# Performance work log

Hardware: AMD Instinct MI355X
Metric: run time of the kernel (lower is better)

## Reference

```python
import jax, jax.numpy as jnp
import numpy as np
from jax import lax

B, C, H, W = 8, 64, 128, 128
K = 3  # deformable kernel size, padding=1, stride=1


def conv3x3(x, w, b=None):
    # x: [B,Cin,H,W], w: [Cout,Cin,3,3]
    y = lax.conv_general_dilated(x, w, (1, 1), 'SAME',
                                 dimension_numbers=('NCHW', 'OIHW', 'NCHW'))
    if b is not None:
        y = y + b[None, :, None, None]
    return y


def leaky_relu(x, slope=0.1):
    return jnp.where(x >= 0, x, slope * x)


def _bilinear_sample_one(feat, ys, xs):
    # feat: [C,H,W]; ys, xs: [KK,H,W] fractional sample coords (zero outside borders)
    h, w = feat.shape[1], feat.shape[2]
    y0 = jnp.floor(ys)
    x0 = jnp.floor(xs)
    wy = ys - y0  # [KK,H,W]
    wx = xs - x0

    def gather(yi, xi):
        valid = ((yi >= 0) & (yi < h) & (xi >= 0) & (xi < w)).astype(feat.dtype)
        yc = jnp.clip(yi, 0, h - 1).astype(jnp.int32)
        xc = jnp.clip(xi, 0, w - 1).astype(jnp.int32)
        v = feat[:, yc, xc]  # [C,KK,H,W]
        return v * valid[None]

    v00 = gather(y0, x0)
    v01 = gather(y0, x0 + 1)
    v10 = gather(y0 + 1, x0)
    v11 = gather(y0 + 1, x0 + 1)
    top = v00 * (1 - wx)[None] + v01 * wx[None]
    bot = v10 * (1 - wx)[None] + v11 * wx[None]
    return top * (1 - wy)[None] + bot * wy[None]  # [C,KK,H,W]


def deform_conv2d(x, offset, weight):
    # x: [B,Cin,H,W]; offset: [B,2*K*K,H,W] (torchvision order: per-tap (dy,dx));
    # weight: [Cout,Cin,K,K]; stride=1, pad=1, dilation=1, groups=1, no bias.
    b, cin, h, w = x.shape
    kk = K * K
    off = offset.reshape(b, kk, 2, h, w)
    dy, dx = off[:, :, 0], off[:, :, 1]  # [B,KK,H,W]
    hh = jnp.arange(h, dtype=x.dtype)[:, None]
    ww = jnp.arange(w, dtype=x.dtype)[None, :]
    ky = (jnp.arange(kk) // K - 1).astype(x.dtype)[None, :, None, None]
    kx = (jnp.arange(kk) % K - 1).astype(x.dtype)[None, :, None, None]
    ys = hh[None, None] + ky + dy  # [B,KK,H,W]
    xs = ww[None, None] + kx + dx
    sampled = jax.vmap(_bilinear_sample_one)(x, ys, xs)  # [B,Cin,KK,H,W]
    wflat = weight.reshape(weight.shape[0], cin, kk)
    return jnp.einsum('bckhw,ock->bohw', sampled, wflat)


def setup_inputs() -> dict:
    key = jax.random.key(0)
    ks = jax.random.split(key, 7)
    ref_feat = jax.random.normal(ks[0], (B, C, H, W), jnp.float32)
    target_feat = jax.random.normal(ks[1], (B, C, H, W), jnp.float32)
    w1 = jax.random.normal(ks[2], (C, 2 * C, 3, 3), jnp.float32) * 0.02
    b1 = jax.random.normal(ks[3], (C,), jnp.float32) * 0.02
    w2 = jax.random.normal(ks[4], (18, C, 3, 3), jnp.float32) * 0.02
    b2 = jax.random.normal(ks[5], (18,), jnp.float32) * 0.02
    wd = jax.random.normal(ks[6], (C, C, 3, 3), jnp.float32) * 0.05
    return {'ref_feat': ref_feat, 'target_feat': target_feat,
            'w1': w1, 'b1': b1, 'w2': w2, 'b2': b2, 'wd': wd}


def reference(ref_feat, target_feat, w1, b1, w2, b2, wd):
    concat_feat = jnp.concatenate([ref_feat, target_feat], axis=1)  # [B,2C,H,W]
    hmid = leaky_relu(conv3x3(concat_feat, w1, b1), 0.1)
    offset = conv3x3(hmid, w2, b2)  # [B,18,H,W]
    aligned_feat = deform_conv2d(target_feat, offset, wd)  # [B,C,H,W]
    return aligned_feat
```

## Files before the change

### kernel.cpp

```cpp
#include <hip/hip_runtime.h>
#include <hip/hip_fp16.h>

#define HW 128
#define PLANE (HW * HW)

typedef __attribute__((ext_vector_type(8))) _Float16 f16x8;
typedef __attribute__((ext_vector_type(4))) float f32x4;

__device__ __forceinline__ unsigned short f2h(float f) {
  return __half_as_ushort(__float2half(f));
}

__device__ __forceinline__ void tile_from_bid_512(int bid, int& b, int& by, int& bx) {
  int wg = (bid & 7) * 64 + (bid >> 3);
  b = wg >> 6;
  int t = wg & 63;
  by = (t >> 3) << 4;
  bx = (t & 7) << 4;
}

__global__ __launch_bounds__(256) void pack_all_kernel(
    const float* __restrict__ w1, const float* __restrict__ w2,
    const float* __restrict__ wd, unsigned short* __restrict__ w1p,
    unsigned short* __restrict__ w2p, unsigned short* __restrict__ wdp) {
  int idx = blockIdx.x * 256 + threadIdx.x;
  if (idx < 73728) {
    int k = idx >> 6, n = idx & 63;
    int tap = k >> 7, ic = k & 127;
    w1p[((k >> 3) * 64 + n) * 8 + (k & 7)] = f2h(w1[(n * 128 + ic) * 9 + tap]);
  } else if (idx < 73728 + 18432) {
    int i = idx - 73728;
    int k = i >> 5, n = i & 31;
    int tap = k >> 6, ic = k & 63;
    float v = (n < 18) ? w2[(n * 64 + ic) * 9 + tap] : 0.f;
    w2p[((k >> 3) * 32 + n) * 8 + (k & 7)] = f2h(v);
  } else if (idx < 73728 + 18432 + 36864) {
    int i = idx - 73728 - 18432;
    int k = i >> 6, n = i & 63;
    int tap = k >> 6, ic = k & 63;
    wdp[((k >> 3) * 64 + n) * 8 + (k & 7)] = f2h(wd[(n * 64 + ic) * 9 + tap]);
  }
}

__global__ __launch_bounds__(256) void to_nhwc_kernel(
    const float* __restrict__ ref, const float* __restrict__ tgt,
    unsigned short* __restrict__ xref, unsigned short* __restrict__ xtgt) {
  __shared__ unsigned short lds[32][136];
  const int b = blockIdx.z, y = blockIdx.y, x0 = blockIdx.x * 32;
  for (int idx = threadIdx.x; idx < 4096; idx += 256) {
    int ic = idx >> 5, px = idx & 31;
    const float* src = (ic < 64) ? ref : tgt;
    lds[px][ic] = f2h(src[(b * 64 + (ic & 63)) * PLANE + y * HW + x0 + px]);
  }
  __syncthreads();
  for (int idx = threadIdx.x; idx < 512; idx += 256) {
    int px = idx >> 4, g = idx & 15;
    uint4 v = *(const uint4*)&lds[px][g * 8];
    size_t base = ((size_t)(b * HW + y) * HW + x0 + px) * 64;
    if (g < 8)
      *(uint4*)(xref + base + g * 8) = v;
    else
      *(uint4*)(xtgt + base + (g - 8) * 8) = v;
  }
}

__device__ __forceinline__ uint4 blend4(uint4 a, uint4 b, uint4 c, uint4 d,
                                        __half2 h00, __half2 h01, __half2 h10, __half2 h11) {
  union U { uint4 u; __half2 h[4]; };
  U A, B, C, D, R;
  A.u = a; B.u = b; C.u = c; D.u = d;
#pragma unroll
  for (int i = 0; i < 4; ++i)
    R.h[i] = __hfma2(D.h[i], h11, __hfma2(C.h[i], h10, __hfma2(B.h[i], h01, __hmul2(A.h[i], h00))));
  return R.u;
}

__global__ __launch_bounds__(512, 2) void mega_kernel(
    const unsigned short* __restrict__ xref, const unsigned short* __restrict__ xtgt,
    const unsigned short* __restrict__ w1p, const float* __restrict__ b1,
    const unsigned short* __restrict__ w2p, const float* __restrict__ b2,
    const unsigned short* __restrict__ wdp, float* __restrict__ out) {
  __shared__ __align__(16) unsigned short bufA[400 * 64];
  __shared__ __align__(16) unsigned short bufB[400 * 64];
  __shared__ float offsL[256 * 20];

  int b, by, bx;
  tile_from_bid_512(blockIdx.x, b, by, bx);
  const int tid = threadIdx.x, lane = tid & 63, w = tid >> 6;
  const int l15 = lane & 15, lg = lane >> 4;

  const unsigned short* rb = xref + (size_t)b * PLANE * 64;
  const unsigned short* tb = xtgt + (size_t)b * PLANE * 64;

  for (int i = tid; i < 3200; i += 512) {
    int rec = i >> 3, g = i & 7;
    int wy = rec / 20, wx = rec - wy * 20;
    int gy = by - 2 + wy, gx = bx - 2 + wx;
    uint4 va = make_uint4(0u, 0u, 0u, 0u), vb = va;
    if ((unsigned)gy < 128u && (unsigned)gx < 128u) {
      size_t o = ((size_t)gy * HW + gx) * 64 + g * 8;
      va = *(const uint4*)(rb + o);
      vb = *(const uint4*)(tb + o);
    }
    int sw = rec * 64 + ((g * 8) ^ ((rec & 7) << 3));
    *(uint4*)(bufA + sw) = va;
    *(uint4*)(bufB + sw) = vb;
  }
  __syncthreads();

  int pyv[3], pxv[3];
#pragma unroll
  for (int n = 0; n < 3; ++n) {
    int p = (w * 3 + n) * 16 + l15;
    p = min(p, 323);
    pyv[n] = p / 18;
    pxv[n] = p - pyv[n] * 18;
  }

  f32x4 acc1[4][3];
#pragma unroll
  for (int mf = 0; mf < 4; ++mf)
#pragma unroll
    for (int n = 0; n < 3; ++n) acc1[mf][n] = (f32x4){0.f, 0.f, 0.f, 0.f};

  for (int c = 0; c < 2; ++c) {
    const unsigned short* src = c ? bufB : bufA;
#pragma unroll
    for (int tap = 0; tap < 9; ++tap) {
      const int ty = tap / 3, tx = tap - ty * 3;
#pragma unroll
      for (int ks = 0; ks < 2; ++ks) {
        f16x8 bp[3];
#pragma unroll
        for (int n = 0; n < 3; ++n) {
          int rec = (pyv[n] + ty) * 20 + pxv[n] + tx;
          bp[n] = *(const f16x8*)(src + rec * 64 + ((ks * 32 + lg * 8) ^ ((rec & 7) << 3)));
        }
        const int kb = tap * 16 + c * 8 + ks * 4 + lg;
        f16x8 aw[4];
#pragma unroll
        for (int mf = 0; mf < 4; ++mf)
          aw[mf] = *(const f16x8*)(w1p + (kb * 64 + mf * 16 + l15) * 8);
#pragma unroll
        for (int mf = 0; mf < 4; ++mf)
#pragma unroll
          for (int n = 0; n < 3; ++n)
            acc1[mf][n] = __builtin_amdgcn_mfma_f32_16x16x32_f16(aw[mf], bp[n], acc1[mf][n], 0, 0, 0);
      }
    }
  }
  __syncthreads();

  unsigned short* hmidL = bufA;
#pragma unroll
  for (int mf = 0; mf < 4; ++mf) {
    const float4 bv = ((const float4*)b1)[mf * 4 + lg];
#pragma unroll
    for (int n = 0; n < 3; ++n) {
      const int p = (w * 3 + n) * 16 + l15;
      const bool valid = ((unsigned)(by - 1 + pyv[n]) < 128u) &&
                         ((unsigned)(bx - 1 + pxv[n]) < 128u);
      const float m = valid ? 1.f : 0.f;
      float v0 = acc1[mf][n][0] + bv.x;
      float v1 = acc1[mf][n][1] + bv.y;
      float v2 = acc1[mf][n][2] + bv.z;
      float v3 = acc1[mf][n][3] + bv.w;
      v0 = ((v0 >= 0.f) ? v0 : 0.1f * v0) * m;
      v1 = ((v1 >= 0.f) ? v1 : 0.1f * v1) * m;
      v2 = ((v2 >= 0.f) ? v2 : 0.1f * v2) * m;
      v3 = ((v3 >= 0.f) ? v3 : 0.1f * v3) * m;
      ushort4 s;
      s.x = f2h(v0); s.y = f2h(v1); s.z = f2h(v2); s.w = f2h(v3);
      const int oc = mf * 16 + lg * 4;
      *(ushort4*)(hmidL + p * 64 + (oc ^ ((p & 7) << 3))) = s;
    }
  }
  __syncthreads();

  f32x4 acc2[2][2];
#pragma unroll
  for (int q = 0; q < 2; ++q)
#pragma unroll
    for (int nf = 0; nf < 2; ++nf) acc2[q][nf] = (f32x4){0.f, 0.f, 0.f, 0.f};

#pragma unroll
  for (int tap = 0; tap < 9; ++tap) {
    const int ty = tap / 3, tx = tap - ty * 3;
#pragma unroll
    for (int ks = 0; ks < 2; ++ks) {
      f16x8 ap[2];
#pragma unroll
      for (int q = 0; q < 2; ++q) {
        int p = (w * 2 + q + ty) * 18 + l15 + tx;
        ap[q] = *(const f16x8*)(hmidL + p * 64 + ((ks * 32 + lg * 8) ^ ((p & 7) << 3)));
      }
      const int kb = tap * 8 + ks * 4 + lg;
      f16x8 bw[2];
#pragma unroll
      for (int nf = 0; nf < 2; ++nf)
        bw[nf] = *(const f16x8*)(w2p + (kb * 32 + nf * 16 + l15) * 8);
#pragma unroll
      for (int q = 0; q < 2; ++q)
#pragma unroll
        for (int nf = 0; nf < 2; ++nf)
          acc2[q][nf] = __builtin_amdgcn_mfma_f32_16x16x32_f16(ap[q], bw[nf], acc2[q][nf], 0, 0, 0);
    }
  }
#pragma unroll
  for (int nf = 0; nf < 2; ++nf) {
    const int oc = nf * 16 + l15;
    if (oc < 18) {
      const float bias = b2[oc];
#pragma unroll
      for (int q = 0; q < 2; ++q)
#pragma unroll
        for (int reg = 0; reg < 4; ++reg) {
          int px = (w * 2 + q) * 16 + lg * 4 + reg;
          offsL[px * 20 + oc] = acc2[q][nf][reg] + bias;
        }
    }
  }
  __syncthreads();

  f32x4 acc[2][4];
#pragma unroll
  for (int q = 0; q < 2; ++q)
#pragma unroll
    for (int nf = 0; nf < 4; ++nf) acc[q][nf] = (f32x4){0.f, 0.f, 0.f, 0.f};

  const int x = bx + l15;

  for (int kk = 0; kk < 9; ++kk) {
    const int kdy = kk / 3 - 1, kdx = kk - (kk / 3) * 3 - 1;
    f16x8 af[2][2];
#pragma unroll
    for (int q = 0; q < 2; ++q) {
      const int y = by + w * 2 + q;
      const int px_lin = (w * 2 + q) * 16 + l15;
      float dy = offsL[px_lin * 20 + kk * 2];
      float dx = offsL[px_lin * 20 + kk * 2 + 1];
      float ys = (float)(y + kdy) + dy;
      float xs = (float)(x + kdx) + dx;
      float y0f = floorf(ys), x0f = floorf(xs);
      float wy = ys - y0f, wx = xs - x0f;
      int y0 = (int)y0f, x0i = (int)x0f;
      int y1 = y0 + 1, x1 = x0i + 1;
      float vy0 = (y0 >= 0 && y0 < HW) ? 1.f : 0.f;
      float vy1 = (y1 >= 0 && y1 < HW) ? 1.f : 0.f;
      float vx0 = (x0i >= 0 && x0i < HW) ? 1.f : 0.f;
      float vx1 = (x1 >= 0 && x1 < HW) ? 1.f : 0.f;
      int y0c = min(max(y0, 0), HW - 1), y1c = min(max(y1, 0), HW - 1);
      int x0c = min(max(x0i, 0), HW - 1), x1c = min(max(x1, 0), HW - 1);
      __half2 h00 = __float2half2_rn((1.f - wy) * (1.f - wx) * vy0 * vx0);
      __half2 h01 = __float2half2_rn((1.f - wy) * wx * vy0 * vx1);
      __half2 h10 = __float2half2_rn(wy * (1.f - wx) * vy1 * vx0);
      __half2 h11 = __float2half2_rn(wy * wx * vy1 * vx1);

      const int wy0 = y0c - by + 2, wy1 = y1c - by + 2;
      const int wx0 = x0c - bx + 2, wx1 = x1c - bx + 2;
      const bool inw = ((unsigned)wy0 < 20u) && ((unsigned)wy1 < 20u) &&
                       ((unsigned)wx0 < 20u) && ((unsigned)wx1 < 20u);
      uint4 c00[2], c01[2], c10[2], c11[2];
      if (inw) {
        const int r00 = wy0 * 20 + wx0, r01 = wy0 * 20 + wx1;
        const int r10 = wy1 * 20 + wx0, r11 = wy1 * 20 + wx1;
#pragma unroll
        for (int ks = 0; ks < 2; ++ks) {
          const int ko = (ks * 32 + lg * 8);
          c00[ks] = *(const uint4*)(bufB + r00 * 64 + (ko ^ ((r00 & 7) << 3)));
          c01[ks] = *(const uint4*)(bufB + r01 * 64 + (ko ^ ((r01 & 7) << 3)));
          c10[ks] = *(const uint4*)(bufB + r10 * 64 + (ko ^ ((r10 & 7) << 3)));
          c11[ks] = *(const uint4*)(bufB + r11 * 64 + (ko ^ ((r11 & 7) << 3)));
        }
      } else {
        const unsigned short* p00 = tb + (y0c * HW + x0c) * 64 + lg * 8;
        const unsigned short* p01 = tb + (y0c * HW + x1c) * 64 + lg * 8;
        const unsigned short* p10 = tb + (y1c * HW + x0c) * 64 + lg * 8;
        const unsigned short* p11 = tb + (y1c * HW + x1c) * 64 + lg * 8;
#pragma unroll
        for (int ks = 0; ks < 2; ++ks) {
          c00[ks] = *(const uint4*)(p00 + ks * 32);
          c01[ks] = *(const uint4*)(p01 + ks * 32);
          c10[ks] = *(const uint4*)(p10 + ks * 32);
          c11[ks] = *(const uint4*)(p11 + ks * 32);
        }
      }
#pragma unroll
      for (int ks = 0; ks < 2; ++ks) {
        uint4 r = blend4(c00[ks], c01[ks], c10[ks], c11[ks], h00, h01, h10, h11);
        af[q][ks] = *(const f16x8*)&r;
      }
    }

#pragma unroll
    for (int ks = 0; ks < 2; ++ks) {
      const int kb = kk * 8 + ks * 4 + lg;
      f16x8 bw[4];
#pragma unroll
      for (int nf = 0; nf < 4; ++nf)
        bw[nf] = *(const f16x8*)(wdp + (kb * 64 + nf * 16 + l15) * 8);
#pragma unroll
      for (int q = 0; q < 2; ++q)
#pragma unroll
        for (int nf = 0; nf < 4; ++nf)
          acc[q][nf] = __builtin_amdgcn_mfma_f32_16x16x32_f16(af[q][ks], bw[nf], acc[q][nf], 0, 0, 0);
    }
  }

  const int px0 = bx + lg * 4;
#pragma unroll
  for (int q = 0; q < 2; ++q) {
    const int py = by + w * 2 + q;
#pragma unroll
    for (int nf = 0; nf < 4; ++nf) {
      const int oc = nf * 16 + l15;
      float4 o;
      o.x = acc[q][nf][0];
      o.y = acc[q][nf][1];
      o.z = acc[q][nf][2];
      o.w = acc[q][nf][3];
      *(float4*)(out + (size_t)(b * 64 + oc) * PLANE + py * HW + px0) = o;
    }
  }
}

extern "C" void kernel_launch(void* const* d_in, const int* in_sizes, int n_in,
                              void* d_out, int out_size, void* d_ws, size_t ws_size,
                              hipStream_t stream) {
  const float* ref = (const float*)d_in[0];
  const float* tgt = (const float*)d_in[1];
  const float* w1  = (const float*)d_in[2];
  const float* b1  = (const float*)d_in[3];
  const float* w2  = (const float*)d_in[4];
  const float* b2  = (const float*)d_in[5];
  const float* wd  = (const float*)d_in[6];
  float* out = (float*)d_out;

  char* ws = (char*)d_ws;
  unsigned short* xref = (unsigned short*)ws;
  unsigned short* xtgt = (unsigned short*)(ws + 16777216);
  unsigned short* w1p  = (unsigned short*)(ws + 33554432);
  unsigned short* w2p  = (unsigned short*)(ws + 33701888);
  unsigned short* wdp  = (unsigned short*)(ws + 33738752);

  pack_all_kernel<<<504, 256, 0, stream>>>(w1, w2, wd, w1p, w2p, wdp);

  to_nhwc_kernel<<<dim3(4, 128, 8), 256, 0, stream>>>(ref, tgt, xref, xtgt);

  mega_kernel<<<512, 512, 0, stream>>>(xref, xtgt, w1p, b1, w2p, b2, wdp, out);
}
```

Measured before the change: 105.7 us.

## Use single padded LDS window buffer, restage target tile, raise occupancy

Replaces the two swizzled 64-channel LDS windows with one padded-stride buffer that is restaged three times: target for the second conv1 half, ref for the first half, then target again for the deformable sampling. LDS per block drops from about 120 KB to about 80 KB, and launch bounds ask for 4 blocks per CU so more waves can overlap. The cost is extra global loads and barriers for the restaging, and a tighter register budget at 512x4 that may spill the large MFMA accumulator arrays. XOR swizzles are replaced by stride padding (72 halves, 22 floats), and offset reads become float2.

```diff
diff --git a/kernel.cpp b/kernel.cpp
--- a/kernel.cpp
+++ b/kernel.cpp
@@ -3,6 +3,8 @@
 
 #define HW 128
 #define PLANE (HW * HW)
+#define WSTR 72
+#define OSTR 22
 
 typedef __attribute__((ext_vector_type(8))) _Float16 f16x8;
 typedef __attribute__((ext_vector_type(4))) float f32x4;
@@ -75,14 +77,13 @@
   return R.u;
 }
 
-__global__ __launch_bounds__(512, 2) void mega_kernel(
+__global__ __launch_bounds__(512, 4) void mega_kernel(
     const unsigned short* __restrict__ xref, const unsigned short* __restrict__ xtgt,
     const unsigned short* __restrict__ w1p, const float* __restrict__ b1,
     const unsigned short* __restrict__ w2p, const float* __restrict__ b2,
     const unsigned short* __restrict__ wdp, float* __restrict__ out) {
-  __shared__ __align__(16) unsigned short bufA[400 * 64];
-  __shared__ __align__(16) unsigned short bufB[400 * 64];
-  __shared__ float offsL[256 * 20];
+  __shared__ __align__(16) unsigned short bufW[400 * WSTR];
+  __shared__ __align__(8) float offsL[256 * OSTR];
 
   int b, by, bx;
   tile_from_bid_512(blockIdx.x, b, by, bx);
@@ -92,21 +93,17 @@
   const unsigned short* rb = xref + (size_t)b * PLANE * 64;
   const unsigned short* tb = xtgt + (size_t)b * PLANE * 64;
 
-  for (int i = tid; i < 3200; i += 512) {
-    int rec = i >> 3, g = i & 7;
-    int wy = rec / 20, wx = rec - wy * 20;
-    int gy = by - 2 + wy, gx = bx - 2 + wx;
-    uint4 va = make_uint4(0u, 0u, 0u, 0u), vb = va;
-    if ((unsigned)gy < 128u && (unsigned)gx < 128u) {
-      size_t o = ((size_t)gy * HW + gx) * 64 + g * 8;
-      va = *(const uint4*)(rb + o);
-      vb = *(const uint4*)(tb + o);
-    }
-    int sw = rec * 64 + ((g * 8) ^ ((rec & 7) << 3));
-    *(uint4*)(bufA + sw) = va;
-    *(uint4*)(bufB + sw) = vb;
-  }
-  __syncthreads();
+  auto STAGE = [&](const unsigned short* src) {
+    for (int i = tid; i < 3200; i += 512) {
+      int rec = i >> 3, g = i & 7;
+      int wy = rec / 20, wx = rec - wy * 20;
+      int gy = by - 2 + wy, gx = bx - 2 + wx;
+      uint4 v = make_uint4(0u, 0u, 0u, 0u);
+      if ((unsigned)gy < 128u && (unsigned)gx < 128u)
+        v = *(const uint4*)(src + ((size_t)gy * HW + gx) * 64 + g * 8);
+      *(uint4*)(bufW + rec * WSTR + g * 8) = v;
+    }
+  };
 
   int pyv[3], pxv[3];
 #pragma unroll
@@ -123,8 +120,7 @@
 #pragma unroll
     for (int n = 0; n < 3; ++n) acc1[mf][n] = (f32x4){0.f, 0.f, 0.f, 0.f};
 
-  for (int c = 0; c < 2; ++c) {
-    const unsigned short* src = c ? bufB : bufA;
+  auto CONV1_HALF = [&](int c) {
 #pragma unroll
     for (int tap = 0; tap < 9; ++tap) {
       const int ty = tap / 3, tx = tap - ty * 3;
@@ -134,7 +130,7 @@
 #pragma unroll
         for (int n = 0; n < 3; ++n) {
           int rec = (pyv[n] + ty) * 20 + pxv[n] + tx;
-          bp[n] = *(const f16x8*)(src + rec * 64 + ((ks * 32 + lg * 8) ^ ((rec & 7) << 3)));
+          bp[n] = *(const f16x8*)(bufW + rec * WSTR + ks * 32 + lg * 8);
         }
         const int kb = tap * 16 + c * 8 + ks * 4 + lg;
         f16x8 aw[4];
@@ -148,10 +144,18 @@
             acc1[mf][n] = __builtin_amdgcn_mfma_f32_16x16x32_f16(aw[mf], bp[n], acc1[mf][n], 0, 0, 0);
       }
     }
-  }
-  __syncthreads();
-
-  unsigned short* hmidL = bufA;
+  };
+
+  STAGE(tb);
+  __syncthreads();
+  CONV1_HALF(1);
+  __syncthreads();
+  STAGE(rb);
+  __syncthreads();
+  CONV1_HALF(0);
+  __syncthreads();
+
+  unsigned short* hmidL = bufW;
 #pragma unroll
   for (int mf = 0; mf < 4; ++mf) {
     const float4 bv = ((const float4*)b1)[mf * 4 + lg];
@@ -171,8 +175,7 @@
       v3 = ((v3 >= 0.f) ? v3 : 0.1f * v3) * m;
       ushort4 s;
       s.x = f2h(v0); s.y = f2h(v1); s.z = f2h(v2); s.w = f2h(v3);
-      const int oc = mf * 16 + lg * 4;
-      *(ushort4*)(hmidL + p * 64 + (oc ^ ((p & 7) << 3))) = s;
+      *(ushort4*)(hmidL + p * WSTR + mf * 16 + lg * 4) = s;
     }
   }
   __syncthreads();
@@ -192,7 +195,7 @@
 #pragma unroll
       for (int q = 0; q < 2; ++q) {
         int p = (w * 2 + q + ty) * 18 + l15 + tx;
-        ap[q] = *(const f16x8*)(hmidL + p * 64 + ((ks * 32 + lg * 8) ^ ((p & 7) << 3)));
+        ap[q] = *(const f16x8*)(hmidL + p * WSTR + ks * 32 + lg * 8);
       }
       const int kb = tap * 8 + ks * 4 + lg;
       f16x8 bw[2];
@@ -216,10 +219,13 @@
 #pragma unroll
         for (int reg = 0; reg < 4; ++reg) {
           int px = (w * 2 + q) * 16 + lg * 4 + reg;
-          offsL[px * 20 + oc] = acc2[q][nf][reg] + bias;
+          offsL[px * OSTR + oc] = acc2[q][nf][reg] + bias;
         }
     }
   }
+  __syncthreads();
+
+  STAGE(tb);
   __syncthreads();
 
   f32x4 acc[2][4];
@@ -237,10 +243,9 @@
     for (int q = 0; q < 2; ++q) {
       const int y = by + w * 2 + q;
       const int px_lin = (w * 2 + q) * 16 + l15;
-      float dy = offsL[px_lin * 20 + kk * 2];
-      float dx = offsL[px_lin * 20 + kk * 2 + 1];
-      float ys = (float)(y + kdy) + dy;
-      float xs = (float)(x + kdx) + dx;
+      const float2 o2 = *(const float2*)(&offsL[px_lin * OSTR + kk * 2]);
+      float ys = (float)(y + kdy) + o2.x;
+      float xs = (float)(x + kdx) + o2.y;
       float y0f = floorf(ys), x0f = floorf(xs);
       float wy = ys - y0f, wx = xs - x0f;
       int y0 = (int)y0f, x0i = (int)x0f;
@@ -266,11 +271,11 @@
         const int r10 = wy1 * 20 + wx0, r11 = wy1 * 20 + wx1;
 #pragma unroll
         for (int ks = 0; ks < 2; ++ks) {
-          const int ko = (ks * 32 + lg * 8);
-          c00[ks] = *(const uint4*)(bufB + r00 * 64 + (ko ^ ((r00 & 7) << 3)));
-          c01[ks] = *(const uint4*)(bufB + r01 * 64 + (ko ^ ((r01 & 7) << 3)));
-          c10[ks] = *(const uint4*)(bufB + r10 * 64 + (ko ^ ((r10 & 7) << 3)));
-          c11[ks] = *(const uint4*)(bufB + r11 * 64 + (ko ^ ((r11 & 7) << 3)));
+          const int ko = ks * 32 + lg * 8;
+          c00[ks] = *(const uint4*)(bufW + r00 * WSTR + ko);
+          c01[ks] = *(const uint4*)(bufW + r01 * WSTR + ko);
+          c10[ks] = *(const uint4*)(bufW + r10 * WSTR + ko);
+          c11[ks] = *(const uint4*)(bufW + r11 * WSTR + ko);
         }
       } else {
         const unsigned short* p00 = tb + (y0c * HW + x0c) * 64 + lg * 8;
```

Measured after the change: 91.06 us. 13.8% less time.
